# Kernel tuning notes

Hardware: AMD Instinct MI355X
Metric: run time of the kernel (lower is better)

The kernel has to match this reference:

```python
import jax, jax.numpy as jnp
import numpy as np

UNITS = 1024
VOCAB = 50000
EMB = 512
SEQ = 256
BATCH = 256


def setup_inputs() -> dict:
    key = jax.random.key(0)
    ks = jax.random.split(key, 9)
    s = lambda fan_in: 1.0 / np.sqrt(fan_in)
    return {
        "sentences": jax.random.randint(ks[0], (BATCH, SEQ), 0, VOCAB),
        "emb_table": jax.random.normal(ks[1], (VOCAB, EMB), jnp.float32) * 0.05,
        # gate order: i, f, g(cell candidate), o
        "Wx": jax.random.normal(ks[2], (EMB, 4 * UNITS), jnp.float32) * s(EMB),
        "Wh": jax.random.normal(ks[3], (UNITS, 4 * UNITS), jnp.float32) * s(UNITS),
        "b": jnp.zeros((4 * UNITS,), jnp.float32),
        "W1": jax.random.normal(ks[4], (UNITS, 64), jnp.float32) * s(UNITS),
        "b1": jnp.zeros((64,), jnp.float32),
        "W2": jax.random.normal(ks[5], (64, 1), jnp.float32) * s(64),
        "b2": jnp.zeros((1,), jnp.float32),
    }


def _lstm_forward(emb_x, Wx, Wh, b):
    # emb_x: [B, T, E] -> final hidden state [B, U]
    B = emb_x.shape[0]
    U = Wh.shape[0]
    # precompute input projections for all timesteps: [T, B, 4U]
    x_proj = jnp.einsum('bte,eg->tbg', emb_x, Wx) + b

    def step(carry, xp):
        h, c = carry
        gates = xp + h @ Wh  # [B, 4U]
        i, f, g, o = jnp.split(gates, 4, axis=-1)
        i = jax.nn.sigmoid(i)
        f = jax.nn.sigmoid(f)
        g = jnp.tanh(g)
        o = jax.nn.sigmoid(o)
        c = f * c + i * g
        h = o * jnp.tanh(c)
        return (h, c), None

    h0 = jnp.zeros((B, U), emb_x.dtype)
    c0 = jnp.zeros((B, U), emb_x.dtype)
    (h, _), _ = jax.lax.scan(step, (h0, c0), x_proj)
    return h


def reference(sentences, emb_table, Wx, Wh, b, W1, b1, W2, b2):
    emb_x = emb_table[sentences]           # [B, T, E]
    h = _lstm_forward(emb_x, Wx, Wh, b)    # [B, U]
    hidden = h @ W1 + b1                   # Dense(64), linear activation
    logits = hidden @ W2 + b2              # Dense(1)
    return jax.nn.sigmoid(logits)          # [B, 1]
```

## Files before the change

### kernel.cpp

```cpp
#include <hip/hip_runtime.h>

#define B_ 256
#define T_ 256
#define E_ 512
#define U_ 1024
#define G_ 4096
#define V_ 50000
#define TC_ 32
#define NCH_ 8
#define NG_ 8
#define NS_ 32
#define CPAD_ 32

typedef __bf16 bf16x8 __attribute__((ext_vector_type(8)));
typedef float f32x4 __attribute__((ext_vector_type(4)));
typedef unsigned short us8 __attribute__((ext_vector_type(8)));
typedef unsigned long long u64x2 __attribute__((ext_vector_type(2)));

__device__ __forceinline__ unsigned short f2bf(float f) {
  union { float f; unsigned u; } v; v.f = f;
  unsigned u = v.u;
  u = (u + 0x7FFFu + ((u >> 16) & 1u)) >> 16;
  return (unsigned short)u;
}
__device__ __forceinline__ float bf2f(unsigned short h) {
  union { unsigned u; float f; } v; v.u = ((unsigned)h) << 16;
  return v.f;
}
__device__ __forceinline__ float sigm_(float x) { return 1.f / (1.f + __expf(-x)); }
__device__ __forceinline__ float tanh_(float x) { return 2.f / (1.f + __expf(-2.f * x)) - 1.f; }

__device__ __forceinline__ void gload16(const void* g, void* l) {
  __builtin_amdgcn_global_load_lds((const __attribute__((address_space(1))) void*)g,
                                   (__attribute__((address_space(3))) void*)l, 16, 0, 0);
}

__device__ __forceinline__ int orig_col3(int p) {
  return (((p >> 5) & 3) << 10) + ((p >> 7) << 5) + (p & 31);
}

__global__ void cvt_bf16_kernel(const float* __restrict__ in, unsigned short* __restrict__ out, long n) {
  long i = (((long)blockIdx.x * blockDim.x) + threadIdx.x) << 3;
  long stride = ((long)gridDim.x * blockDim.x) << 3;
  for (; i < n; i += stride) {
    float4 x = *(const float4*)(in + i);
    float4 y = *(const float4*)(in + i + 4);
    us8 v;
    v[0] = f2bf(x.x); v[1] = f2bf(x.y); v[2] = f2bf(x.z); v[3] = f2bf(x.w);
    v[4] = f2bf(y.x); v[5] = f2bf(y.y); v[6] = f2bf(y.z); v[7] = f2bf(y.w);
    *(us8*)(out + i) = v;
  }
}

__global__ void pack_wx_kernel(const float* __restrict__ w, unsigned short* __restrict__ out, int total) {
  int t = blockIdx.x * blockDim.x + threadIdx.x;
  if (t >= total) return;
  int kb = t >> 12, n = t & 4095;
  int oc = orig_col3(n);
  us8 v;
#pragma unroll
  for (int ki = 0; ki < 8; ki++) v[ki] = f2bf(w[(size_t)(kb * 8 + ki) * G_ + oc]);
  *(us8*)(out + (size_t)t * 8) = v;
}

__global__ void pack_wh3_kernel(const float* __restrict__ w, unsigned short* __restrict__ out) {
  int t = blockIdx.x * blockDim.x + threadIdx.x;
  int lane = t & 63;
  int nf = (t >> 6) & 1;
  int ks = (t >> 7) & 15;
  int nq = (t >> 11) & 3;
  int kh = (t >> 13) & 1;
  int s  = t >> 14;
  int k0 = kh * 512 + ks * 32 + (lane >> 4) * 8;
  int oc = nq * 1024 + s * 32 + nf * 16 + (lane & 15);
  us8 v;
#pragma unroll
  for (int i = 0; i < 8; i++) v[i] = f2bf(w[(size_t)(k0 + i) * G_ + oc]);
  *(us8*)(out + (size_t)t * 8) = v;
}

#define XP_BM 128
#define XP_BN 128
#define XP_KC 64
__global__ __launch_bounds__(256, 2) void xproj_kernel(
    const int* __restrict__ sent, const unsigned short* __restrict__ embb,
    const unsigned short* __restrict__ wxp, const float* __restrict__ bias,
    unsigned short* __restrict__ xp, int t0)
{
  __shared__ __align__(16) unsigned short sA[2][XP_BM * XP_KC];
  __shared__ __align__(16) unsigned short sB[2][XP_KC * XP_BN];
  __shared__ int tok[XP_BM];

  const int tid = threadIdx.x;
  const int lane = tid & 63;
  const int wid = tid >> 6;
  const int m0 = blockIdx.x * XP_BM;
  const int n0 = blockIdx.y * XP_BN;

  if (tid < XP_BM) {
    int row = m0 + tid;
    int tl = row >> 8, b = row & 255;
    tok[tid] = sent[b * T_ + t0 + tl];
  }
  __syncthreads();

  auto stageA = [&](int bf, int kc) {
#pragma unroll
    for (int ii = 0; ii < 4; ii++) {
      int i = wid * 4 + ii;
      int m = i * 8 + (lane >> 3);
      int cl = lane & 7;
      const unsigned short* src = embb + (size_t)tok[m] * E_ + kc + ((cl ^ (m & 7)) << 3);
      gload16(src, &sA[bf][i * 512]);
    }
  };
  auto stageB = [&](int bf, int kc) {
    int kb0 = kc >> 3;
#pragma unroll
    for (int jj = 0; jj < 4; jj++) {
      int j = wid * 4 + jj;
      int r = j >> 1;
      int nl = ((j & 1) << 6) + lane;
      int n = nl ^ r;
      const unsigned short* src = wxp + ((size_t)(kb0 + r) * G_ + n0 + n) * 8;
      gload16(src, &sB[bf][j * 512]);
    }
  };

  f32x4 acc[4][4];
#pragma unroll
  for (int i = 0; i < 4; i++)
#pragma unroll
    for (int j = 0; j < 4; j++) acc[i][j] = f32x4{0.f, 0.f, 0.f, 0.f};

  const int wm = wid >> 1, wn = wid & 1;

  stageA(0, 0); stageB(0, 0);
  for (int it = 0; it < E_ / XP_KC; it++) {
    int bf = it & 1;
    __syncthreads();
    if (it < E_ / XP_KC - 1) { stageA(bf ^ 1, (it + 1) * XP_KC); stageB(bf ^ 1, (it + 1) * XP_KC); }
#pragma unroll
    for (int kk = 0; kk < 2; kk++) {
      int c = (kk << 2) + (lane >> 4);
      bf16x8 a[4], b[4];
#pragma unroll
      for (int ms = 0; ms < 4; ms++) {
        int m = (wm << 6) + (ms << 4) + (lane & 15);
        a[ms] = *(const bf16x8*)&sA[bf][m * 64 + ((c ^ (m & 7)) << 3)];
      }
#pragma unroll
      for (int ns = 0; ns < 4; ns++) {
        int n = (wn << 6) + (ns << 4) + (lane & 15);
        b[ns] = *(const bf16x8*)&sB[bf][((c << 7) + (n ^ c)) << 3];
      }
#pragma unroll
      for (int ms = 0; ms < 4; ms++)
#pragma unroll
        for (int ns = 0; ns < 4; ns++)
          acc[ms][ns] = __builtin_amdgcn_mfma_f32_16x16x32_bf16(a[ms], b[ns], acc[ms][ns], 0, 0, 0);
    }
  }

#pragma unroll
  for (int ns = 0; ns < 4; ns++) {
    int col = n0 + (wn << 6) + (ns << 4) + (lane & 15);
    float bv = bias[orig_col3(col)];
#pragma unroll
    for (int ms = 0; ms < 4; ms++) {
      int rbase = m0 + (wm << 6) + (ms << 4) + ((lane >> 4) << 2);
#pragma unroll
      for (int rr = 0; rr < 4; rr++)
        xp[(size_t)(rbase + rr) * G_ + col] = f2bf(acc[ms][ns][rr] + bv);
    }
  }
}

__global__ __launch_bounds__(512, 2) void scan_kernel(
    const unsigned short* __restrict__ xpc,
    const unsigned short* __restrict__ whp3,
    unsigned short* __restrict__ hbuf,
    float* __restrict__ cst,
    int* __restrict__ cnt,
    int t0)
{
  __shared__ __align__(16) unsigned short sA[32 * 1024];
  __shared__ float sG[4][32][33];
  __shared__ float sP[4][32][33];

  const int tid = threadIdx.x, lane = tid & 63, w = tid >> 6;
  const int kh = w >> 2, nq = w & 3;
  const int g = (int)blockIdx.x & 7, s = (int)blockIdx.x >> 3;
  const int m0g = g * 32;
  const int u0 = s * 32;
  const int rx = lane & 7;

  bf16x8 wh[16][2];
  {
    const bf16x8* wb = (const bf16x8*)whp3 +
        (((((size_t)s * 2 + kh) * 4 + nq) * 16) * 2) * 64;
#pragma unroll
    for (int ks = 0; ks < 16; ks++)
#pragma unroll
      for (int nf = 0; nf < 2; nf++)
        wh[ks][nf] = wb[(ks * 2 + nf) * 64 + lane];
  }

  const int r_e = tid >> 4, ue = (tid & 15) * 2;
  const size_t ci = (size_t)(m0g + r_e) * U_ + u0 + ue;
  float c0v = cst[ci], c1v = cst[ci + 1];

  const int sr0 = tid >> 7;
  const int sc = tid & 127;

  const char* sAb = (const char*)sA;
  const char* abase0 = sAb + (size_t)(lane & 15) * 2048 + kh * 1024;
  const char* abase1 = abase0 + 16 * 2048;

  for (int ts = 0; ts < TC_; ts++) {
    const int t = t0 + ts;
    if (t > 0) {
      if (tid == 0) {
        int* cp = cnt + (size_t)(t * NG_ + g) * CPAD_;
        while (__hip_atomic_load(cp, __ATOMIC_RELAXED, __HIP_MEMORY_SCOPE_AGENT) < NS_) {}
      }
      __syncthreads();
    }

    const unsigned short* hsrc = hbuf + (size_t)(t & 1) * (B_ * U_) + (size_t)m0g * U_;
#pragma unroll
    for (int jj = 0; jj < 2; jj++) {
      unsigned long long hv[4][2];
#pragma unroll
      for (int j = 0; j < 4; j++) {
        int r = (jj * 4 + j) * 4 + sr0;
        unsigned long long* p = (unsigned long long*)(hsrc + (size_t)r * U_ + sc * 8);
        hv[j][0] = __hip_atomic_load(p, __ATOMIC_RELAXED, __HIP_MEMORY_SCOPE_AGENT);
        hv[j][1] = __hip_atomic_load(p + 1, __ATOMIC_RELAXED, __HIP_MEMORY_SCOPE_AGENT);
      }
#pragma unroll
      for (int j = 0; j < 4; j++) {
        int r = (jj * 4 + j) * 4 + sr0;
        u64x2 v; v[0] = hv[j][0]; v[1] = hv[j][1];
        *(u64x2*)((char*)sAb + (size_t)r * 2048 + ((sc ^ (r & 7)) << 4)) = v;
      }
    }
    __syncthreads();

    f32x4 acc[2][2];
#pragma unroll
    for (int i = 0; i < 2; i++) { acc[i][0] = f32x4{0.f,0.f,0.f,0.f}; acc[i][1] = f32x4{0.f,0.f,0.f,0.f}; }
#pragma unroll
    for (int ks = 0; ks < 16; ks++) {
      int c = ks * 4 + (lane >> 4);
      bf16x8 a0 = *(const bf16x8*)(abase0 + ((c ^ rx) << 4));
      bf16x8 a1 = *(const bf16x8*)(abase1 + ((c ^ rx) << 4));
      acc[0][0] = __builtin_amdgcn_mfma_f32_16x16x32_bf16(a0, wh[ks][0], acc[0][0], 0, 0, 0);
      acc[0][1] = __builtin_amdgcn_mfma_f32_16x16x32_bf16(a0, wh[ks][1], acc[0][1], 0, 0, 0);
      acc[1][0] = __builtin_amdgcn_mfma_f32_16x16x32_bf16(a1, wh[ks][0], acc[1][0], 0, 0, 0);
      acc[1][1] = __builtin_amdgcn_mfma_f32_16x16x32_bf16(a1, wh[ks][1], acc[1][1], 0, 0, 0);
    }

    const unsigned short* xr = xpc + ((size_t)ts * B_ + (m0g + r_e)) * G_ + s * 128;
    unsigned xiv = *(const unsigned*)(xr + ue);
    unsigned xfv = *(const unsigned*)(xr + 32 + ue);
    unsigned xgv = *(const unsigned*)(xr + 64 + ue);
    unsigned xov = *(const unsigned*)(xr + 96 + ue);

    {
      float (*sOut)[32][33] = kh ? sP : sG;
#pragma unroll
      for (int mt = 0; mt < 2; mt++)
#pragma unroll
        for (int nf = 0; nf < 2; nf++)
#pragma unroll
          for (int rr = 0; rr < 4; rr++)
            sOut[nq][mt * 16 + (lane >> 4) * 4 + rr][nf * 16 + (lane & 15)] = acc[mt][nf][rr];
    }
    __syncthreads();

    {
      float cn[2]; unsigned hv = 0;
#pragma unroll
      for (int j = 0; j < 2; j++) {
        int u = ue + j;
        float gi = sG[0][r_e][u] + sP[0][r_e][u] + bf2f((unsigned short)(j ? (xiv >> 16) : xiv));
        float gf = sG[1][r_e][u] + sP[1][r_e][u] + bf2f((unsigned short)(j ? (xfv >> 16) : xfv));
        float gg = sG[2][r_e][u] + sP[2][r_e][u] + bf2f((unsigned short)(j ? (xgv >> 16) : xgv));
        float go = sG[3][r_e][u] + sP[3][r_e][u] + bf2f((unsigned short)(j ? (xov >> 16) : xov));
        float co = j ? c1v : c0v;
        float cv = sigm_(gf) * co + sigm_(gi) * tanh_(gg);
        cn[j] = cv;
        hv |= (unsigned)f2bf(sigm_(go) * tanh_(cv)) << (16 * j);
      }
      c0v = cn[0]; c1v = cn[1];
      unsigned* hdst = (unsigned*)(hbuf + (size_t)((t + 1) & 1) * (B_ * U_) + ci);
      __hip_atomic_store(hdst, hv, __ATOMIC_RELAXED, __HIP_MEMORY_SCOPE_AGENT);
    }
    __syncthreads();
    if (tid == 0)
      __hip_atomic_fetch_add(cnt + (size_t)((t + 1) * NG_ + g) * CPAD_, 1,
                             __ATOMIC_RELAXED, __HIP_MEMORY_SCOPE_AGENT);
  }

  cst[ci] = c0v; cst[ci + 1] = c1v;
}

__global__ __launch_bounds__(256) void dense_kernel(
    const unsigned short* __restrict__ h, const float* __restrict__ W1, const float* __restrict__ b1,
    const float* __restrict__ W2, const float* __restrict__ b2, float* __restrict__ out)
{
  int tid = threadIdx.x, j = tid & 63, kq = tid >> 6;
  const unsigned short* hr = h + (size_t)blockIdx.x * U_;
  float s = 0.f;
#pragma unroll 8
  for (int k = kq * 256; k < kq * 256 + 256; k++) s += bf2f(hr[k]) * W1[k * 64 + j];
  __shared__ float red[4][64];
  red[kq][j] = s;
  __syncthreads();
  if (tid < 64) {
    float hid = red[0][j] + red[1][j] + red[2][j] + red[3][j] + b1[j];
    float p = hid * W2[j];
#pragma unroll
    for (int off = 32; off; off >>= 1) p += __shfl_down(p, off, 64);
    if (j == 0) out[blockIdx.x] = 1.f / (1.f + __expf(-(p + b2[0])));
  }
}

extern "C" void kernel_launch(void* const* d_in, const int* in_sizes, int n_in,
                              void* d_out, int out_size, void* d_ws, size_t ws_size,
                              hipStream_t stream) {
  const int*   sent = (const int*)d_in[0];
  const float* emb  = (const float*)d_in[1];
  const float* Wx   = (const float*)d_in[2];
  const float* Wh   = (const float*)d_in[3];
  const float* bias = (const float*)d_in[4];
  const float* W1   = (const float*)d_in[5];
  const float* b1   = (const float*)d_in[6];
  const float* W2   = (const float*)d_in[7];
  const float* b2   = (const float*)d_in[8];
  float* out = (float*)d_out;

  char* ws = (char*)d_ws;
  size_t off = 0;
  auto alloc = [&](size_t bytes) { void* p = ws + off; off += (bytes + 255) & ~(size_t)255; return p; };
  unsigned short* embb = (unsigned short*)alloc((size_t)V_ * E_ * 2);
  unsigned short* wxp  = (unsigned short*)alloc((size_t)E_ * G_ * 2);
  unsigned short* whp3 = (unsigned short*)alloc((size_t)U_ * G_ * 2);
  unsigned short* xpc  = (unsigned short*)alloc((size_t)TC_ * B_ * G_ * 2);
  unsigned short* hbuf = (unsigned short*)alloc((size_t)2 * B_ * U_ * 2);
  float*          cst  = (float*)alloc((size_t)B_ * U_ * 4);
  int*            cnt  = (int*)alloc((size_t)(T_ + 1) * NG_ * CPAD_ * 4);

  hipLaunchKernelGGL(cvt_bf16_kernel, dim3(12500), dim3(256), 0, stream, emb, embb, (long)V_ * E_);
  hipLaunchKernelGGL(pack_wx_kernel, dim3((E_ / 8) * G_ / 256), dim3(256), 0, stream, Wx, wxp, (E_ / 8) * G_);
  hipLaunchKernelGGL(pack_wh3_kernel, dim3(2048), dim3(256), 0, stream, Wh, whp3);
  hipMemsetAsync(hbuf, 0, (size_t)B_ * U_ * 2, stream);
  hipMemsetAsync(cst, 0, (size_t)B_ * U_ * 4, stream);
  hipMemsetAsync(cnt, 0, (size_t)(T_ + 1) * NG_ * CPAD_ * 4, stream);

  for (int ch = 0; ch < NCH_; ch++) {
    hipLaunchKernelGGL(xproj_kernel, dim3(TC_ * B_ / XP_BM, G_ / XP_BN), dim3(256), 0, stream,
                       sent, embb, wxp, bias, xpc, ch * TC_);
    hipLaunchKernelGGL(scan_kernel, dim3(NG_ * NS_), dim3(512), 0, stream,
                       xpc, whp3, hbuf, cst, cnt, ch * TC_);
  }
  hipLaunchKernelGGL(dense_kernel, dim3(B_), dim3(256), 0, stream,
                     hbuf , W1, b1, W2, b2, out);
}
```

Measured before the change: 1.657 ms.

## Fuse input projection of next chunk with recurrent scan in one persistent launch

Merges the xproj and scan kernels into one 512-block launch. Blocks 0-255 run the recurrent LSTM steps for the current chunk while blocks 256-511 compute the input projection for the next chunk into a double buffer, so the projection GEMM overlaps the latency-bound scan. The h-state load now goes global-to-LDS directly, and chunk size drops to 16 steps with 16 launches. The risks are that the xproj blocks compete with the scan blocks for CUs and bandwidth, that there are more launches, and that the scan blocks depend on spin-waits that assume all of them are co-resident. The h store also changes from an atomic store to a plain store.

```diff
diff --git a/kernel.cpp b/kernel.cpp
--- a/kernel.cpp
+++ b/kernel.cpp
@@ -6,8 +6,8 @@
 #define U_ 1024
 #define G_ 4096
 #define V_ 50000
-#define TC_ 32
-#define NCH_ 8
+#define TC_ 16
+#define NCH_ 16
 #define NG_ 8
 #define NS_ 32
 #define CPAD_ 32
@@ -15,7 +15,6 @@
 typedef __bf16 bf16x8 __attribute__((ext_vector_type(8)));
 typedef float f32x4 __attribute__((ext_vector_type(4)));
 typedef unsigned short us8 __attribute__((ext_vector_type(8)));
-typedef unsigned long long u64x2 __attribute__((ext_vector_type(2)));
 
 __device__ __forceinline__ unsigned short f2bf(float f) {
   union { float f; unsigned u; } v; v.f = f;
@@ -33,6 +32,10 @@
 __device__ __forceinline__ void gload16(const void* g, void* l) {
   __builtin_amdgcn_global_load_lds((const __attribute__((address_space(1))) void*)g,
                                    (__attribute__((address_space(3))) void*)l, 16, 0, 0);
+}
+__device__ __forceinline__ void gload16c(const void* g, void* l) {
+  __builtin_amdgcn_global_load_lds((const __attribute__((address_space(1))) void*)g,
+                                   (__attribute__((address_space(3))) void*)l, 16, 0, 1);
 }
 
 __device__ __forceinline__ int orig_col3(int p) {
@@ -110,8 +113,7 @@
       int i = wid * 4 + ii;
       int m = i * 8 + (lane >> 3);
       int cl = lane & 7;
-      const unsigned short* src = embb + (size_t)tok[m] * E_ + kc + ((cl ^ (m & 7)) << 3);
-      gload16(src, &sA[bf][i * 512]);
+      gload16(embb + (size_t)tok[m] * E_ + kc + ((cl ^ (m & 7)) << 3), &sA[bf][i * 512]);
     }
   };
   auto stageB = [&](int bf, int kc) {
@@ -122,8 +124,7 @@
       int r = j >> 1;
       int nl = ((j & 1) << 6) + lane;
       int n = nl ^ r;
-      const unsigned short* src = wxp + ((size_t)(kb0 + r) * G_ + n0 + n) * 8;
-      gload16(src, &sB[bf][j * 512]);
+      gload16(wxp + ((size_t)(kb0 + r) * G_ + n0 + n) * 8, &sB[bf][j * 512]);
     }
   };
 
@@ -176,134 +177,210 @@
   }
 }
 
-__global__ __launch_bounds__(512, 2) void scan_kernel(
-    const unsigned short* __restrict__ xpc,
+__global__ __launch_bounds__(512) void fused_kernel(
+    const int* __restrict__ sent, const unsigned short* __restrict__ embb,
+    const unsigned short* __restrict__ wxp, const float* __restrict__ bias,
+    unsigned short* __restrict__ xpc0, unsigned short* __restrict__ xpc1,
     const unsigned short* __restrict__ whp3,
-    unsigned short* __restrict__ hbuf,
-    float* __restrict__ cst,
-    int* __restrict__ cnt,
-    int t0)
+    unsigned short* __restrict__ hbuf, float* __restrict__ cst,
+    int* __restrict__ cnt, int ch)
 {
-  __shared__ __align__(16) unsigned short sA[32 * 1024];
-  __shared__ float sG[4][32][33];
-  __shared__ float sP[4][32][33];
-
+  __shared__ __align__(16) char smem[66048];
   const int tid = threadIdx.x, lane = tid & 63, w = tid >> 6;
-  const int kh = w >> 2, nq = w & 3;
-  const int g = (int)blockIdx.x & 7, s = (int)blockIdx.x >> 3;
-  const int m0g = g * 32;
-  const int u0 = s * 32;
-  const int rx = lane & 7;
-
-  bf16x8 wh[16][2];
-  {
-    const bf16x8* wb = (const bf16x8*)whp3 +
-        (((((size_t)s * 2 + kh) * 4 + nq) * 16) * 2) * 64;
-#pragma unroll
-    for (int ks = 0; ks < 16; ks++)
-#pragma unroll
-      for (int nf = 0; nf < 2; nf++)
-        wh[ks][nf] = wb[(ks * 2 + nf) * 64 + lane];
-  }
-
-  const int r_e = tid >> 4, ue = (tid & 15) * 2;
-  const size_t ci = (size_t)(m0g + r_e) * U_ + u0 + ue;
-  float c0v = cst[ci], c1v = cst[ci + 1];
-
-  const int sr0 = tid >> 7;
-  const int sc = tid & 127;
-
-  const char* sAb = (const char*)sA;
-  const char* abase0 = sAb + (size_t)(lane & 15) * 2048 + kh * 1024;
-  const char* abase1 = abase0 + 16 * 2048;
-
-  for (int ts = 0; ts < TC_; ts++) {
-    const int t = t0 + ts;
-    if (t > 0) {
-      if (tid == 0) {
-        int* cp = cnt + (size_t)(t * NG_ + g) * CPAD_;
-        while (__hip_atomic_load(cp, __ATOMIC_RELAXED, __HIP_MEMORY_SCOPE_AGENT) < NS_) {}
-      }
-      __syncthreads();
-    }
-
-    const unsigned short* hsrc = hbuf + (size_t)(t & 1) * (B_ * U_) + (size_t)m0g * U_;
-#pragma unroll
-    for (int jj = 0; jj < 2; jj++) {
-      unsigned long long hv[4][2];
-#pragma unroll
-      for (int j = 0; j < 4; j++) {
-        int r = (jj * 4 + j) * 4 + sr0;
-        unsigned long long* p = (unsigned long long*)(hsrc + (size_t)r * U_ + sc * 8);
-        hv[j][0] = __hip_atomic_load(p, __ATOMIC_RELAXED, __HIP_MEMORY_SCOPE_AGENT);
-        hv[j][1] = __hip_atomic_load(p + 1, __ATOMIC_RELAXED, __HIP_MEMORY_SCOPE_AGENT);
-      }
-#pragma unroll
-      for (int j = 0; j < 4; j++) {
-        int r = (jj * 4 + j) * 4 + sr0;
-        u64x2 v; v[0] = hv[j][0]; v[1] = hv[j][1];
-        *(u64x2*)((char*)sAb + (size_t)r * 2048 + ((sc ^ (r & 7)) << 4)) = v;
-      }
-    }
-    __syncthreads();
-
-    f32x4 acc[2][2];
-#pragma unroll
-    for (int i = 0; i < 2; i++) { acc[i][0] = f32x4{0.f,0.f,0.f,0.f}; acc[i][1] = f32x4{0.f,0.f,0.f,0.f}; }
-#pragma unroll
-    for (int ks = 0; ks < 16; ks++) {
-      int c = ks * 4 + (lane >> 4);
-      bf16x8 a0 = *(const bf16x8*)(abase0 + ((c ^ rx) << 4));
-      bf16x8 a1 = *(const bf16x8*)(abase1 + ((c ^ rx) << 4));
-      acc[0][0] = __builtin_amdgcn_mfma_f32_16x16x32_bf16(a0, wh[ks][0], acc[0][0], 0, 0, 0);
-      acc[0][1] = __builtin_amdgcn_mfma_f32_16x16x32_bf16(a0, wh[ks][1], acc[0][1], 0, 0, 0);
-      acc[1][0] = __builtin_amdgcn_mfma_f32_16x16x32_bf16(a1, wh[ks][0], acc[1][0], 0, 0, 0);
-      acc[1][1] = __builtin_amdgcn_mfma_f32_16x16x32_bf16(a1, wh[ks][1], acc[1][1], 0, 0, 0);
-    }
-
-    const unsigned short* xr = xpc + ((size_t)ts * B_ + (m0g + r_e)) * G_ + s * 128;
-    unsigned xiv = *(const unsigned*)(xr + ue);
-    unsigned xfv = *(const unsigned*)(xr + 32 + ue);
-    unsigned xgv = *(const unsigned*)(xr + 64 + ue);
-    unsigned xov = *(const unsigned*)(xr + 96 + ue);
-
+
+  if (blockIdx.x < 256) {
+    unsigned short* sA = (unsigned short*)smem;
+    float* sEx = (float*)smem;
+    const unsigned short* xin = (ch & 1) ? xpc1 : xpc0;
+    const int t0 = ch * TC_;
+    const int kh = w >> 2, nq = w & 3;
+    const int g = (int)blockIdx.x & 7, s = (int)blockIdx.x >> 3;
+    const int m0g = g * 32, u0 = s * 32;
+    const int rx = lane & 7;
+
+    bf16x8 wh[16][2];
     {
-      float (*sOut)[32][33] = kh ? sP : sG;
-#pragma unroll
-      for (int mt = 0; mt < 2; mt++)
+      const bf16x8* wb = (const bf16x8*)whp3 + (((size_t)s * 2 + kh) * 4 + nq) * 32 * 64;
+#pragma unroll
+      for (int ks = 0; ks < 16; ks++)
 #pragma unroll
         for (int nf = 0; nf < 2; nf++)
+          wh[ks][nf] = wb[(ks * 2 + nf) * 64 + lane];
+    }
+
+    const int r_e = tid >> 4, ue = (tid & 15) * 2;
+    const size_t ci = (size_t)(m0g + r_e) * U_ + u0 + ue;
+    float c0v = cst[ci], c1v = cst[ci + 1];
+
+    const char* abase0 = smem + (size_t)(lane & 15) * 2048 + kh * 1024;
+    const char* abase1 = abase0 + 16 * 2048;
+
+    for (int ts = 0; ts < TC_; ts++) {
+      const int t = t0 + ts;
+      if (t > 0) {
+        if (tid == 0) {
+          const int* cp = cnt + (size_t)(t * NG_ + g) * CPAD_;
+          while (__hip_atomic_load(cp, __ATOMIC_RELAXED, __HIP_MEMORY_SCOPE_AGENT) < NS_) {}
+        }
+        __syncthreads();
+      }
+
+      const unsigned short* hsrc = hbuf + (size_t)(t & 1) * (B_ * U_) + (size_t)m0g * U_;
+#pragma unroll
+      for (int jj = 0; jj < 8; jj++) {
+        int j = w * 8 + jj;
+        int r = j >> 1, k2 = j & 1;
+        gload16c(hsrc + (size_t)r * U_ + (((k2 << 6) | (lane ^ (r & 7))) << 3),
+                 &sA[r * 1024 + k2 * 512]);
+      }
+      __syncthreads();
+
+      f32x4 acc[2][2];
+#pragma unroll
+      for (int i = 0; i < 2; i++) { acc[i][0] = f32x4{0.f,0.f,0.f,0.f}; acc[i][1] = f32x4{0.f,0.f,0.f,0.f}; }
+#pragma unroll
+      for (int ks = 0; ks < 16; ks++) {
+        int c = ks * 4 + (lane >> 4);
+        bf16x8 a0 = *(const bf16x8*)(abase0 + ((c ^ rx) << 4));
+        bf16x8 a1 = *(const bf16x8*)(abase1 + ((c ^ rx) << 4));
+        acc[0][0] = __builtin_amdgcn_mfma_f32_16x16x32_bf16(a0, wh[ks][0], acc[0][0], 0, 0, 0);
+        acc[0][1] = __builtin_amdgcn_mfma_f32_16x16x32_bf16(a0, wh[ks][1], acc[0][1], 0, 0, 0);
+        acc[1][0] = __builtin_amdgcn_mfma_f32_16x16x32_bf16(a1, wh[ks][0], acc[1][0], 0, 0, 0);
+        acc[1][1] = __builtin_amdgcn_mfma_f32_16x16x32_bf16(a1, wh[ks][1], acc[1][1], 0, 0, 0);
+      }
+
+      const unsigned short* xr = xin + ((size_t)ts * B_ + (m0g + r_e)) * G_ + s * 128;
+      unsigned xiv = *(const unsigned*)(xr + ue);
+      unsigned xfv = *(const unsigned*)(xr + 32 + ue);
+      unsigned xgv = *(const unsigned*)(xr + 64 + ue);
+      unsigned xov = *(const unsigned*)(xr + 96 + ue);
+
+      __syncthreads();
+
+      {
+        float* sOut = sEx + (kh ? 4224 : 0);
+#pragma unroll
+        for (int mt = 0; mt < 2; mt++)
+#pragma unroll
+          for (int nf = 0; nf < 2; nf++)
+#pragma unroll
+            for (int rr = 0; rr < 4; rr++)
+              sOut[(nq * 32 + mt * 16 + (lane >> 4) * 4 + rr) * 33 + nf * 16 + (lane & 15)] = acc[mt][nf][rr];
+      }
+      __syncthreads();
+
+      {
+        float cn[2]; unsigned hv = 0;
+#pragma unroll
+        for (int j = 0; j < 2; j++) {
+          int u = ue + j;
+          float gi = sEx[(0 * 32 + r_e) * 33 + u] + sEx[4224 + (0 * 32 + r_e) * 33 + u] + bf2f((unsigned short)(j ? (xiv >> 16) : xiv));
+          float gf = sEx[(1 * 32 + r_e) * 33 + u] + sEx[4224 + (1 * 32 + r_e) * 33 + u] + bf2f((unsigned short)(j ? (xfv >> 16) : xfv));
+          float gg = sEx[(2 * 32 + r_e) * 33 + u] + sEx[4224 + (2 * 32 + r_e) * 33 + u] + bf2f((unsigned short)(j ? (xgv >> 16) : xgv));
+          float go = sEx[(3 * 32 + r_e) * 33 + u] + sEx[4224 + (3 * 32 + r_e) * 33 + u] + bf2f((unsigned short)(j ? (xov >> 16) : xov));
+          float co = j ? c1v : c0v;
+          float cv = sigm_(gf) * co + sigm_(gi) * tanh_(gg);
+          cn[j] = cv;
+          hv |= (unsigned)f2bf(sigm_(go) * tanh_(cv)) << (16 * j);
+        }
+        c0v = cn[0]; c1v = cn[1];
+        *(unsigned*)(hbuf + (size_t)((t + 1) & 1) * (B_ * U_) + ci) = hv;
+      }
+      __syncthreads();
+      if (tid == 0)
+        __hip_atomic_fetch_add(cnt + (size_t)((t + 1) * NG_ + g) * CPAD_, 1,
+                               __ATOMIC_RELAXED, __HIP_MEMORY_SCOPE_AGENT);
+    }
+    cst[ci] = c0v; cst[ci + 1] = c1v;
+
+  } else {
+    if (ch + 1 >= NCH_) return;
+    unsigned short (*sAx)[XP_BM * XP_KC] = (unsigned short (*)[XP_BM * XP_KC])smem;
+    unsigned short (*sBx)[XP_KC * XP_BN] = (unsigned short (*)[XP_KC * XP_BN])(smem + 32768);
+    int* tok = (int*)(smem + 65536);
+    unsigned short* xout = ((ch + 1) & 1) ? xpc1 : xpc0;
+    const int t0x = (ch + 1) * TC_;
+    const int q = (int)blockIdx.x - 256;
+    const int wm = w >> 1, wn = w & 1;
+
+    for (int i = 0; i < 4; i++) {
+      int job = q * 4 + i;
+      int m0 = (job >> 5) * XP_BM;
+      int n0 = (job & 31) * XP_BN;
+      __syncthreads();
+      if (tid < XP_BM) {
+        int row = m0 + tid;
+        int tl = row >> 8, b = row & 255;
+        tok[tid] = sent[b * T_ + t0x + tl];
+      }
+      __syncthreads();
+
+      auto stageA = [&](int bf, int kc) {
+#pragma unroll
+        for (int ii = 0; ii < 2; ii++) {
+          int idx = w * 2 + ii;
+          int m = idx * 8 + (lane >> 3), cl = lane & 7;
+          gload16(embb + (size_t)tok[m] * E_ + kc + ((cl ^ (m & 7)) << 3), &sAx[bf][idx * 512]);
+        }
+      };
+      auto stageB = [&](int bf, int kc) {
+        int kb0 = kc >> 3;
+#pragma unroll
+        for (int jj = 0; jj < 2; jj++) {
+          int j = w * 2 + jj;
+          int r = j >> 1;
+          int nl = ((j & 1) << 6) + lane, n = nl ^ r;
+          gload16(wxp + ((size_t)(kb0 + r) * G_ + n0 + n) * 8, &sBx[bf][j * 512]);
+        }
+      };
+
+      f32x4 acc[2][4];
+#pragma unroll
+      for (int ms = 0; ms < 2; ms++)
+#pragma unroll
+        for (int ns = 0; ns < 4; ns++) acc[ms][ns] = f32x4{0.f, 0.f, 0.f, 0.f};
+
+      stageA(0, 0); stageB(0, 0);
+      for (int it = 0; it < E_ / XP_KC; it++) {
+        int bf = it & 1;
+        __syncthreads();
+        if (it < E_ / XP_KC - 1) { stageA(bf ^ 1, (it + 1) * XP_KC); stageB(bf ^ 1, (it + 1) * XP_KC); }
+#pragma unroll
+        for (int kk = 0; kk < 2; kk++) {
+          int c = (kk << 2) + (lane >> 4);
+          bf16x8 a[2], b[4];
+#pragma unroll
+          for (int ms = 0; ms < 2; ms++) {
+            int m = wm * 32 + ms * 16 + (lane & 15);
+            a[ms] = *(const bf16x8*)&sAx[bf][m * 64 + ((c ^ (m & 7)) << 3)];
+          }
+#pragma unroll
+          for (int ns = 0; ns < 4; ns++) {
+            int n = wn * 64 + ns * 16 + (lane & 15);
+            b[ns] = *(const bf16x8*)&sBx[bf][((c << 7) + (n ^ c)) << 3];
+          }
+#pragma unroll
+          for (int ms = 0; ms < 2; ms++)
+#pragma unroll
+            for (int ns = 0; ns < 4; ns++)
+              acc[ms][ns] = __builtin_amdgcn_mfma_f32_16x16x32_bf16(a[ms], b[ns], acc[ms][ns], 0, 0, 0);
+        }
+      }
+
+#pragma unroll
+      for (int ns = 0; ns < 4; ns++) {
+        int col = n0 + wn * 64 + ns * 16 + (lane & 15);
+        float bv = bias[orig_col3(col)];
+#pragma unroll
+        for (int ms = 0; ms < 2; ms++) {
+          int rbase = m0 + wm * 32 + ms * 16 + ((lane >> 4) << 2);
 #pragma unroll
           for (int rr = 0; rr < 4; rr++)
-            sOut[nq][mt * 16 + (lane >> 4) * 4 + rr][nf * 16 + (lane & 15)] = acc[mt][nf][rr];
-    }
-    __syncthreads();
-
-    {
-      float cn[2]; unsigned hv = 0;
-#pragma unroll
-      for (int j = 0; j < 2; j++) {
-        int u = ue + j;
-        float gi = sG[0][r_e][u] + sP[0][r_e][u] + bf2f((unsigned short)(j ? (xiv >> 16) : xiv));
-        float gf = sG[1][r_e][u] + sP[1][r_e][u] + bf2f((unsigned short)(j ? (xfv >> 16) : xfv));
-        float gg = sG[2][r_e][u] + sP[2][r_e][u] + bf2f((unsigned short)(j ? (xgv >> 16) : xgv));
-        float go = sG[3][r_e][u] + sP[3][r_e][u] + bf2f((unsigned short)(j ? (xov >> 16) : xov));
-        float co = j ? c1v : c0v;
-        float cv = sigm_(gf) * co + sigm_(gi) * tanh_(gg);
-        cn[j] = cv;
-        hv |= (unsigned)f2bf(sigm_(go) * tanh_(cv)) << (16 * j);
-      }
-      c0v = cn[0]; c1v = cn[1];
-      unsigned* hdst = (unsigned*)(hbuf + (size_t)((t + 1) & 1) * (B_ * U_) + ci);
-      __hip_atomic_store(hdst, hv, __ATOMIC_RELAXED, __HIP_MEMORY_SCOPE_AGENT);
-    }
-    __syncthreads();
-    if (tid == 0)
-      __hip_atomic_fetch_add(cnt + (size_t)((t + 1) * NG_ + g) * CPAD_, 1,
-                             __ATOMIC_RELAXED, __HIP_MEMORY_SCOPE_AGENT);
-  }
-
-  cst[ci] = c0v; cst[ci + 1] = c1v;
+            xout[(size_t)(rbase + rr) * G_ + col] = f2bf(acc[ms][ns][rr] + bv);
+        }
+      }
+    }
+  }
 }
 
 __global__ __launch_bounds__(256) void dense_kernel(
@@ -347,7 +424,8 @@
   unsigned short* embb = (unsigned short*)alloc((size_t)V_ * E_ * 2);
   unsigned short* wxp  = (unsigned short*)alloc((size_t)E_ * G_ * 2);
   unsigned short* whp3 = (unsigned short*)alloc((size_t)U_ * G_ * 2);
-  unsigned short* xpc  = (unsigned short*)alloc((size_t)TC_ * B_ * G_ * 2);
+  unsigned short* xpc0 = (unsigned short*)alloc((size_t)TC_ * B_ * G_ * 2);
+  unsigned short* xpc1 = (unsigned short*)alloc((size_t)TC_ * B_ * G_ * 2);
   unsigned short* hbuf = (unsigned short*)alloc((size_t)2 * B_ * U_ * 2);
   float*          cst  = (float*)alloc((size_t)B_ * U_ * 4);
   int*            cnt  = (int*)alloc((size_t)(T_ + 1) * NG_ * CPAD_ * 4);
@@ -359,11 +437,12 @@
   hipMemsetAsync(cst, 0, (size_t)B_ * U_ * 4, stream);
   hipMemsetAsync(cnt, 0, (size_t)(T_ + 1) * NG_ * CPAD_ * 4, stream);
 
+  hipLaunchKernelGGL(xproj_kernel, dim3(TC_ * B_ / XP_BM, G_ / XP_BN), dim3(256), 0, stream,
+                     sent, embb, wxp, bias, xpc0, 0);
+
   for (int ch = 0; ch < NCH_; ch++) {
-    hipLaunchKernelGGL(xproj_kernel, dim3(TC_ * B_ / XP_BM, G_ / XP_BN), dim3(256), 0, stream,
-                       sent, embb, wxp, bias, xpc, ch * TC_);
-    hipLaunchKernelGGL(scan_kernel, dim3(NG_ * NS_), dim3(512), 0, stream,
-                       xpc, whp3, hbuf, cst, cnt, ch * TC_);
+    hipLaunchKernelGGL(fused_kernel, dim3(512), dim3(512), 0, stream,
+                       sent, embb, wxp, bias, xpc0, xpc1, whp3, hbuf, cst, cnt, ch);
   }
   hipLaunchKernelGGL(dense_kernel, dim3(B_), dim3(256), 0, stream,
                      hbuf , W1, b1, W2, b2, out);
```

After: 1.691 ms. 2.1% more time.
